# Kernel tuning notes

Measured on AMD Instinct MI355X. Metric: run time of the kernel, lower is better.

## Reference

```python
import jax, jax.numpy as jnp
import numpy as np
from jax import lax

B, N, H, L, K = 16, 2000, 128, 3, 5
LN_EPS = 1e-5


def setup_inputs() -> dict:
    key = jax.random.key(0)
    ks = jax.random.split(key, 4)
    node_emb = jax.random.normal(ks[0], (B, N, H), dtype=jnp.float32)
    dist_matrix = jax.random.uniform(ks[1], (B, N, N), dtype=jnp.float32)
    Ws = jax.random.normal(ks[2], (L, H, H), dtype=jnp.float32) / np.sqrt(H)
    bs = jax.random.normal(ks[3], (L, H), dtype=jnp.float32) * 0.02
    gammas = jnp.ones((L, H), dtype=jnp.float32)
    betas = jnp.zeros((L, H), dtype=jnp.float32)
    return {"node_emb": node_emb, "dist_matrix": dist_matrix,
            "Ws": Ws, "bs": bs, "gammas": gammas, "betas": betas}


def _layer_norm(x, gamma, beta):
    mu = jnp.mean(x, axis=-1, keepdims=True)
    var = jnp.mean(jnp.square(x - mu), axis=-1, keepdims=True)
    return (x - mu) * lax.rsqrt(var + LN_EPS) * gamma + beta


def reference(node_emb, dist_matrix, Ws, bs, gammas, betas):
    # kNN mask: k smallest distances per row (B, N, K)
    _, knn_idx = lax.top_k(-dist_matrix, K)
    b_ix = jnp.arange(B)[:, None, None]
    n_ix = jnp.arange(N)[None, :, None]
    knn_mask = jnp.zeros((B, N, N), dtype=bool).at[b_ix, n_ix, knn_idx].set(True)
    scores = jnp.where(knn_mask, -dist_matrix, -jnp.inf)
    weights = jax.nn.softmax(scores, axis=-1)  # (B, N, N)

    h = node_emb
    for l in range(L):
        agg = jnp.einsum('bnm,bmh->bnh', weights, h)
        delta = jax.nn.relu(agg @ Ws[l].T + bs[l])
        h = _layer_norm(h + delta, gammas[l], betas[l])
    return h
```

## Files before the change

kernel.cpp:

```cpp
#include <hip/hip_runtime.h>
#include <hip/hip_bf16.h>

#define BATCH 16
#define NNODE 2000
#define HDIM  128
#define KNN   5
#define NROWS (BATCH * NNODE)
#define LN_EPS 1e-5f

typedef __attribute__((ext_vector_type(8))) short short8;
typedef __attribute__((ext_vector_type(4))) float f32x4;

__global__ __launch_bounds__(256) void prep_w_kernel(
    const float* __restrict__ Ws, __hip_bfloat16* __restrict__ WB)
{
    int t = blockIdx.x * 256 + threadIdx.x;
    if (t >= 3 * 2048) return;
    int l    = t >> 11;
    int r    = t & 2047;
    int lane = r & 63;
    int ks   = (r >> 6) & 3;
    int ct   = (r >> 8) & 1;
    int wv   = (r >> 9) & 3;
    int col  = wv * 32 + ct * 16 + (lane & 15);
    int k0   = ks * 32 + (lane >> 4) * 8;
    const float* src = Ws + ((size_t)l << 14) + col * HDIM + k0;
    __hip_bfloat16* dst = WB + ((size_t)t << 3);
    #pragma unroll
    for (int e = 0; e < 8; ++e) dst[e] = __float2bfloat16(src[e]);
}

__device__ __forceinline__ unsigned long long pack_di(float v, unsigned int idx) {
    unsigned int b = __float_as_uint(v);
    b = (b & 0x80000000u) ? ~b : (b | 0x80000000u);
    return ((unsigned long long)b << 32) | idx;
}

__global__ __launch_bounds__(256) void knn_softmax_kernel(
    const float* __restrict__ dist,
    int* __restrict__ w_idx,
    float* __restrict__ w_val)
{
    int row  = blockIdx.x * 4 + (threadIdx.x >> 6);
    int lane = threadIdx.x & 63;
    const float4* r4 = reinterpret_cast<const float4*>(dist + (size_t)row * NNODE);

    unsigned long long pk0 = ~0ull, pk1 = ~0ull, pk2 = ~0ull, pk3 = ~0ull, pk4 = ~0ull;

    auto ins = [&](float d, int m) {
        unsigned long long key = pack_di(d, (unsigned int)m);
        if (key < pk4) {
            pk4 = key;
            unsigned long long t;
            if (pk4 < pk3) { t = pk3; pk3 = pk4; pk4 = t; }
            if (pk3 < pk2) { t = pk2; pk2 = pk3; pk3 = t; }
            if (pk2 < pk1) { t = pk1; pk1 = pk2; pk2 = t; }
            if (pk1 < pk0) { t = pk0; pk0 = pk1; pk1 = t; }
        }
    };

    float4 v[8];
    int base7 = lane + 448;
    bool has8 = base7 < (NNODE / 4);
    #pragma unroll
    for (int i = 0; i < 7; ++i) v[i] = r4[lane + 64 * i];
    v[7] = r4[has8 ? base7 : lane];

    #pragma unroll
    for (int i = 0; i < 7; ++i) {
        int base = (lane + 64 * i) * 4;
        ins(v[i].x, base); ins(v[i].y, base + 1);
        ins(v[i].z, base + 2); ins(v[i].w, base + 3);
    }
    if (has8) {
        int base = base7 * 4;
        ins(v[7].x, base); ins(v[7].y, base + 1);
        ins(v[7].z, base + 2); ins(v[7].w, base + 3);
    }

    unsigned long long chosen[KNN];
    #pragma unroll
    for (int r = 0; r < KNN; ++r) {
        unsigned long long mn = pk0;
        #pragma unroll
        for (int off = 32; off; off >>= 1) {
            unsigned long long o = __shfl_xor(mn, off, 64);
            if (o < mn) mn = o;
        }
        if (pk0 == mn) { pk0 = pk1; pk1 = pk2; pk2 = pk3; pk3 = pk4; pk4 = ~0ull; }
        chosen[r] = mn;
    }

    if (lane == 0) {
        float d[KNN]; int ix[KNN];
        #pragma unroll
        for (int r = 0; r < KNN; ++r) {
            unsigned int ub = (unsigned int)(chosen[r] >> 32);
            ub = (ub & 0x80000000u) ? (ub ^ 0x80000000u) : ~ub;
            d[r]  = __uint_as_float(ub);
            ix[r] = (int)(chosen[r] & 0xffffffffu);
        }
        float e[KNN]; float sum = 0.f;
        #pragma unroll
        for (int r = 0; r < KNN; ++r) { e[r] = expf(d[0] - d[r]); sum += e[r]; }
        float inv = 1.f / sum;
        #pragma unroll
        for (int r = 0; r < KNN; ++r) {
            w_idx[row * KNN + r] = ix[r];
            w_val[row * KNN + r] = e[r] * inv;
        }
    }
}

__global__ __launch_bounds__(256) void layer_kernel(
    const float* __restrict__ h_in,
    const int*   __restrict__ w_idx,
    const float* __restrict__ w_val,
    const __hip_bfloat16* __restrict__ WB,
    const float* __restrict__ bias,
    const float* __restrict__ gamma,
    const float* __restrict__ beta,
    float* __restrict__ h_out)
{
    __shared__ __hip_bfloat16 aggb[16][HDIM];
    __shared__ int   sidx[16][KNN];
    __shared__ float sw[16][KNN];
    __shared__ float wred[4][16][2];

    int tid = threadIdx.x;
    int wv  = tid >> 6;
    int l   = tid & 63;

    int bid = blockIdx.x;
    int x   = bid & 7;
    int j   = bid >> 3;
    int hi  = (j >= 125);
    int bsw = 2 * x + hi;
    int gid = bsw * 125 + (j - hi * 125);

    int node0 = gid * 16;
    size_t hbase = (size_t)bsw * NNODE * HDIM;

    const short8* wb = reinterpret_cast<const short8*>(WB);
    short8 bfrag[2][4];
    #pragma unroll
    for (int ct = 0; ct < 2; ++ct)
        #pragma unroll
        for (int ks = 0; ks < 4; ++ks)
            bfrag[ct][ks] = wb[((wv * 2 + ct) * 4 + ks) * 64 + l];

    if (tid < 16 * KNN) {
        int m = tid / KNN, k = tid % KNN;
        sidx[m][k] = w_idx[(node0 + m) * KNN + k];
        sw[m][k]   = w_val[(node0 + m) * KNN + k];
    }
    __syncthreads();

    {
        int m  = tid >> 4;
        int c0 = (tid & 15) * 8;
        float a0=0,a1=0,a2=0,a3=0,a4=0,a5=0,a6=0,a7=0;
        #pragma unroll
        for (int k = 0; k < KNN; ++k) {
            float wk = sw[m][k];
            const float4* p = reinterpret_cast<const float4*>(
                h_in + hbase + (size_t)sidx[m][k] * HDIM + c0);
            float4 v0 = p[0], v1 = p[1];
            a0 = fmaf(wk, v0.x, a0); a1 = fmaf(wk, v0.y, a1);
            a2 = fmaf(wk, v0.z, a2); a3 = fmaf(wk, v0.w, a3);
            a4 = fmaf(wk, v1.x, a4); a5 = fmaf(wk, v1.y, a5);
            a6 = fmaf(wk, v1.z, a6); a7 = fmaf(wk, v1.w, a7);
        }
        float vv[8] = {a0,a1,a2,a3,a4,a5,a6,a7};
        short8 pk;
        #pragma unroll
        for (int e = 0; e < 8; ++e) {
            __hip_bfloat16 hb = __float2bfloat16(vv[e]);
            pk[e] = *reinterpret_cast<short*>(&hb);
        }
        *reinterpret_cast<short8*>(&aggb[m][c0]) = pk;
    }
    __syncthreads();

    f32x4 acc0 = {0.f,0.f,0.f,0.f}, acc1 = {0.f,0.f,0.f,0.f};
    #pragma unroll
    for (int ks = 0; ks < 4; ++ks) {
        short8 afrag = *reinterpret_cast<const short8*>(&aggb[l & 15][ks * 32 + (l >> 4) * 8]);
        acc0 = __builtin_amdgcn_mfma_f32_16x16x32_bf16(afrag, bfrag[0][ks], acc0, 0, 0, 0);
        acc1 = __builtin_amdgcn_mfma_f32_16x16x32_bf16(afrag, bfrag[1][ks], acc1, 0, 0, 0);
    }

    int g = l >> 4;
    int col0 = wv * 32 + (l & 15);
    int col1 = col0 + 16;
    float b0  = bias[col0],  b1  = bias[col1];
    float gm0 = gamma[col0], gm1 = gamma[col1];
    float bt0 = beta[col0],  bt1 = beta[col1];

    float y0[4], y1[4];
    #pragma unroll
    for (int r = 0; r < 4; ++r) {
        int row = node0 + g * 4 + r;
        float h0 = h_in[(size_t)row * HDIM + col0];
        float h1 = h_in[(size_t)row * HDIM + col1];
        y0[r] = h0 + fmaxf(acc0[r] + b0, 0.f);
        y1[r] = h1 + fmaxf(acc1[r] + b1, 0.f);
    }

    #pragma unroll
    for (int r = 0; r < 4; ++r) {
        float ss = y0[r] + y1[r];
        float qq = y0[r] * y0[r] + y1[r] * y1[r];
        #pragma unroll
        for (int off = 1; off < 16; off <<= 1) {
            ss += __shfl_xor(ss, off, 64);
            qq += __shfl_xor(qq, off, 64);
        }
        if ((l & 15) == 0) { wred[wv][g * 4 + r][0] = ss; wred[wv][g * 4 + r][1] = qq; }
    }
    __syncthreads();

    #pragma unroll
    for (int r = 0; r < 4; ++r) {
        int row = g * 4 + r;
        float S = wred[0][row][0] + wred[1][row][0] + wred[2][row][0] + wred[3][row][0];
        float Q = wred[0][row][1] + wred[1][row][1] + wred[2][row][1] + wred[3][row][1];
        float mu  = S * (1.f / 128.f);
        float var = Q * (1.f / 128.f) - mu * mu;
        float rs  = rsqrtf(var + LN_EPS);
        size_t orow = (size_t)(node0 + row) * HDIM;
        h_out[orow + col0] = (y0[r] - mu) * rs * gm0 + bt0;
        h_out[orow + col1] = (y1[r] - mu) * rs * gm1 + bt1;
    }
}

extern "C" void kernel_launch(void* const* d_in, const int* in_sizes, int n_in,
                              void* d_out, int out_size, void* d_ws, size_t ws_size,
                              hipStream_t stream) {
    const float* node_emb = (const float*)d_in[0];
    const float* dist     = (const float*)d_in[1];
    const float* Ws       = (const float*)d_in[2];
    const float* bs       = (const float*)d_in[3];
    const float* gammas   = (const float*)d_in[4];
    const float* betas    = (const float*)d_in[5];
    float* out = (float*)d_out;

    char* ws = (char*)d_ws;
    int*   w_idx = (int*)  (ws + 0);
    float* w_val = (float*)(ws + 640000);
    __hip_bfloat16* WB = (__hip_bfloat16*)(ws + 1280000);
    float* h_mid = (float*)(ws + 1378304);

    prep_w_kernel<<<24, 256, 0, stream>>>(Ws, WB);
    knn_softmax_kernel<<<NROWS / 4, 256, 0, stream>>>(dist, w_idx, w_val);

    const int nblocks = NROWS / 16;
    const int WL = 16384;
    layer_kernel<<<nblocks, 256, 0, stream>>>(node_emb, w_idx, w_val,
        WB,          bs,           gammas,           betas,           out);
    layer_kernel<<<nblocks, 256, 0, stream>>>(out,      w_idx, w_val,
        WB + WL,     bs + HDIM,    gammas + HDIM,    betas + HDIM,    h_mid);
    layer_kernel<<<nblocks, 256, 0, stream>>>(h_mid,    w_idx, w_val,
        WB + 2*WL,   bs + 2*HDIM,  gammas + 2*HDIM,  betas + 2*HDIM,  out);
}
```

Before: 110.3 us.

## Fuse kNN softmax selection into first layer kernel and stage own rows in LDS

The separate kNN/softmax kernel is merged into the first layer kernel: each block computes top-k weights for its 16 rows, keeps them in shared memory and still writes them out for later layers. This removes one launch and the global round trip of indices and weights before layer 1. The residual rows are also loaded once, coalesced, into shared memory instead of strided global reads in the epilogue. In exchange, each wave now processes four distance rows serially, which may reduce memory parallelism on the dominant distance-matrix read, and shared memory use grows.

```diff
diff --git a/kernel.cpp b/kernel.cpp
--- a/kernel.cpp
+++ b/kernel.cpp
@@ -36,79 +36,199 @@
     return ((unsigned long long)b << 32) | idx;
 }
 
-__global__ __launch_bounds__(256) void knn_softmax_kernel(
+__global__ __launch_bounds__(256) void fused_knn_layer1_kernel(
     const float* __restrict__ dist,
-    int* __restrict__ w_idx,
-    float* __restrict__ w_val)
+    const float* __restrict__ h_in,
+    const __hip_bfloat16* __restrict__ WB0,
+    const float* __restrict__ bias,
+    const float* __restrict__ gamma,
+    const float* __restrict__ beta,
+    int*   __restrict__ w_idx,
+    float* __restrict__ w_val,
+    float* __restrict__ h_out)
 {
-    int row  = blockIdx.x * 4 + (threadIdx.x >> 6);
-    int lane = threadIdx.x & 63;
-    const float4* r4 = reinterpret_cast<const float4*>(dist + (size_t)row * NNODE);
-
-    unsigned long long pk0 = ~0ull, pk1 = ~0ull, pk2 = ~0ull, pk3 = ~0ull, pk4 = ~0ull;
-
-    auto ins = [&](float d, int m) {
-        unsigned long long key = pack_di(d, (unsigned int)m);
-        if (key < pk4) {
-            pk4 = key;
-            unsigned long long t;
-            if (pk4 < pk3) { t = pk3; pk3 = pk4; pk4 = t; }
-            if (pk3 < pk2) { t = pk2; pk2 = pk3; pk3 = t; }
-            if (pk2 < pk1) { t = pk1; pk1 = pk2; pk2 = t; }
-            if (pk1 < pk0) { t = pk0; pk0 = pk1; pk1 = t; }
-        }
-    };
-
-    float4 v[8];
-    int base7 = lane + 448;
-    bool has8 = base7 < (NNODE / 4);
-    #pragma unroll
-    for (int i = 0; i < 7; ++i) v[i] = r4[lane + 64 * i];
-    v[7] = r4[has8 ? base7 : lane];
-
-    #pragma unroll
-    for (int i = 0; i < 7; ++i) {
-        int base = (lane + 64 * i) * 4;
-        ins(v[i].x, base); ins(v[i].y, base + 1);
-        ins(v[i].z, base + 2); ins(v[i].w, base + 3);
-    }
-    if (has8) {
-        int base = base7 * 4;
-        ins(v[7].x, base); ins(v[7].y, base + 1);
-        ins(v[7].z, base + 2); ins(v[7].w, base + 3);
-    }
-
-    unsigned long long chosen[KNN];
-    #pragma unroll
-    for (int r = 0; r < KNN; ++r) {
-        unsigned long long mn = pk0;
-        #pragma unroll
-        for (int off = 32; off; off >>= 1) {
-            unsigned long long o = __shfl_xor(mn, off, 64);
-            if (o < mn) mn = o;
-        }
-        if (pk0 == mn) { pk0 = pk1; pk1 = pk2; pk2 = pk3; pk3 = pk4; pk4 = ~0ull; }
-        chosen[r] = mn;
-    }
-
-    if (lane == 0) {
-        float d[KNN]; int ix[KNN];
+    __shared__ __hip_bfloat16 aggb[16][HDIM];
+    __shared__ float hown[16][HDIM];
+    __shared__ int   sidx[16][KNN];
+    __shared__ float sw[16][KNN];
+    __shared__ float wred[4][16][2];
+
+    int tid = threadIdx.x;
+    int wv  = tid >> 6;
+    int l   = tid & 63;
+
+    int bid = blockIdx.x;
+    int x   = bid & 7;
+    int j   = bid >> 3;
+    int hi  = (j >= 125);
+    int bsw = 2 * x + hi;
+    int gid = bsw * 125 + (j - hi * 125);
+
+    int node0 = gid * 16;
+    size_t hbase = (size_t)bsw * NNODE * HDIM;
+
+    for (int rr = 0; rr < 4; ++rr) {
+        int m   = wv * 4 + rr;
+        int row = node0 + m;
+        const float4* r4 = reinterpret_cast<const float4*>(dist + (size_t)row * NNODE);
+
+        unsigned long long pk0=~0ull, pk1=~0ull, pk2=~0ull, pk3=~0ull, pk4=~0ull;
+        auto ins = [&](float d, int mm) {
+            unsigned long long key = pack_di(d, (unsigned int)mm);
+            if (key < pk4) {
+                pk4 = key;
+                unsigned long long t;
+                if (pk4 < pk3) { t = pk3; pk3 = pk4; pk4 = t; }
+                if (pk3 < pk2) { t = pk2; pk2 = pk3; pk3 = t; }
+                if (pk2 < pk1) { t = pk1; pk1 = pk2; pk2 = t; }
+                if (pk1 < pk0) { t = pk0; pk0 = pk1; pk1 = t; }
+            }
+        };
+
+        float4 v[8];
+        int base7 = l + 448;
+        bool has8 = base7 < (NNODE / 4);
+        #pragma unroll
+        for (int i = 0; i < 7; ++i) v[i] = r4[l + 64 * i];
+        v[7] = r4[has8 ? base7 : l];
+
+        #pragma unroll
+        for (int i = 0; i < 7; ++i) {
+            int base = (l + 64 * i) * 4;
+            ins(v[i].x, base); ins(v[i].y, base + 1);
+            ins(v[i].z, base + 2); ins(v[i].w, base + 3);
+        }
+        if (has8) {
+            int base = base7 * 4;
+            ins(v[7].x, base); ins(v[7].y, base + 1);
+            ins(v[7].z, base + 2); ins(v[7].w, base + 3);
+        }
+
+        unsigned long long chosen[KNN];
         #pragma unroll
         for (int r = 0; r < KNN; ++r) {
-            unsigned int ub = (unsigned int)(chosen[r] >> 32);
-            ub = (ub & 0x80000000u) ? (ub ^ 0x80000000u) : ~ub;
-            d[r]  = __uint_as_float(ub);
-            ix[r] = (int)(chosen[r] & 0xffffffffu);
-        }
-        float e[KNN]; float sum = 0.f;
-        #pragma unroll
-        for (int r = 0; r < KNN; ++r) { e[r] = expf(d[0] - d[r]); sum += e[r]; }
-        float inv = 1.f / sum;
-        #pragma unroll
-        for (int r = 0; r < KNN; ++r) {
-            w_idx[row * KNN + r] = ix[r];
-            w_val[row * KNN + r] = e[r] * inv;
-        }
+            unsigned long long mn = pk0;
+            #pragma unroll
+            for (int off = 32; off; off >>= 1) {
+                unsigned long long o = __shfl_xor(mn, off, 64);
+                if (o < mn) mn = o;
+            }
+            if (pk0 == mn) { pk0 = pk1; pk1 = pk2; pk2 = pk3; pk3 = pk4; pk4 = ~0ull; }
+            chosen[r] = mn;
+        }
+
+        if (l == 0) {
+            float d[KNN]; int ix[KNN];
+            #pragma unroll
+            for (int r = 0; r < KNN; ++r) {
+                unsigned int ub = (unsigned int)(chosen[r] >> 32);
+                ub = (ub & 0x80000000u) ? (ub ^ 0x80000000u) : ~ub;
+                d[r]  = __uint_as_float(ub);
+                ix[r] = (int)(chosen[r] & 0xffffffffu);
+            }
+            float e[KNN]; float sum = 0.f;
+            #pragma unroll
+            for (int r = 0; r < KNN; ++r) { e[r] = expf(d[0] - d[r]); sum += e[r]; }
+            float inv = 1.f / sum;
+            #pragma unroll
+            for (int r = 0; r < KNN; ++r) {
+                float wt = e[r] * inv;
+                sidx[m][r] = ix[r];
+                sw[m][r]   = wt;
+                w_idx[row * KNN + r] = ix[r];
+                w_val[row * KNN + r] = wt;
+            }
+        }
+    }
+    __syncthreads();
+
+    const short8* wb = reinterpret_cast<const short8*>(WB0);
+    short8 bfrag[2][4];
+    #pragma unroll
+    for (int ct = 0; ct < 2; ++ct)
+        #pragma unroll
+        for (int ks = 0; ks < 4; ++ks)
+            bfrag[ct][ks] = wb[((wv * 2 + ct) * 4 + ks) * 64 + l];
+
+    {
+        int m  = tid >> 4;
+        int c0 = (tid & 15) * 8;
+        const float4* po = reinterpret_cast<const float4*>(
+            h_in + (size_t)(node0 + m) * HDIM + c0);
+        float4 o0 = po[0], o1 = po[1];
+        *reinterpret_cast<float4*>(&hown[m][c0])     = o0;
+        *reinterpret_cast<float4*>(&hown[m][c0 + 4]) = o1;
+
+        float a0=0,a1=0,a2=0,a3=0,a4=0,a5=0,a6=0,a7=0;
+        #pragma unroll
+        for (int k = 0; k < KNN; ++k) {
+            float wk = sw[m][k];
+            const float4* p = reinterpret_cast<const float4*>(
+                h_in + hbase + (size_t)sidx[m][k] * HDIM + c0);
+            float4 v0 = p[0], v1 = p[1];
+            a0 = fmaf(wk, v0.x, a0); a1 = fmaf(wk, v0.y, a1);
+            a2 = fmaf(wk, v0.z, a2); a3 = fmaf(wk, v0.w, a3);
+            a4 = fmaf(wk, v1.x, a4); a5 = fmaf(wk, v1.y, a5);
+            a6 = fmaf(wk, v1.z, a6); a7 = fmaf(wk, v1.w, a7);
+        }
+        float vv[8] = {a0,a1,a2,a3,a4,a5,a6,a7};
+        short8 pk;
+        #pragma unroll
+        for (int e = 0; e < 8; ++e) {
+            __hip_bfloat16 hb = __float2bfloat16(vv[e]);
+            pk[e] = *reinterpret_cast<short*>(&hb);
+        }
+        *reinterpret_cast<short8*>(&aggb[m][c0]) = pk;
+    }
+    __syncthreads();
+
+    f32x4 acc0 = {0.f,0.f,0.f,0.f}, acc1 = {0.f,0.f,0.f,0.f};
+    #pragma unroll
+    for (int ks = 0; ks < 4; ++ks) {
+        short8 afrag = *reinterpret_cast<const short8*>(&aggb[l & 15][ks * 32 + (l >> 4) * 8]);
+        acc0 = __builtin_amdgcn_mfma_f32_16x16x32_bf16(afrag, bfrag[0][ks], acc0, 0, 0, 0);
+        acc1 = __builtin_amdgcn_mfma_f32_16x16x32_bf16(afrag, bfrag[1][ks], acc1, 0, 0, 0);
+    }
+
+    int g = l >> 4;
+    int col0 = wv * 32 + (l & 15);
+    int col1 = col0 + 16;
+    float b0  = bias[col0],  b1  = bias[col1];
+    float gm0 = gamma[col0], gm1 = gamma[col1];
+    float bt0 = beta[col0],  bt1 = beta[col1];
+
+    float y0[4], y1[4];
+    #pragma unroll
+    for (int r = 0; r < 4; ++r) {
+        int rl = g * 4 + r;
+        y0[r] = hown[rl][col0] + fmaxf(acc0[r] + b0, 0.f);
+        y1[r] = hown[rl][col1] + fmaxf(acc1[r] + b1, 0.f);
+    }
+
+    #pragma unroll
+    for (int r = 0; r < 4; ++r) {
+        float ss = y0[r] + y1[r];
+        float qq = y0[r] * y0[r] + y1[r] * y1[r];
+        #pragma unroll
+        for (int off = 1; off < 16; off <<= 1) {
+            ss += __shfl_xor(ss, off, 64);
+            qq += __shfl_xor(qq, off, 64);
+        }
+        if ((l & 15) == 0) { wred[wv][g * 4 + r][0] = ss; wred[wv][g * 4 + r][1] = qq; }
+    }
+    __syncthreads();
+
+    #pragma unroll
+    for (int r = 0; r < 4; ++r) {
+        int row = g * 4 + r;
+        float S = wred[0][row][0] + wred[1][row][0] + wred[2][row][0] + wred[3][row][0];
+        float Q = wred[0][row][1] + wred[1][row][1] + wred[2][row][1] + wred[3][row][1];
+        float mu  = S * (1.f / 128.f);
+        float var = Q * (1.f / 128.f) - mu * mu;
+        float rs  = rsqrtf(var + LN_EPS);
+        size_t orow = (size_t)(node0 + row) * HDIM;
+        h_out[orow + col0] = (y0[r] - mu) * rs * gm0 + bt0;
+        h_out[orow + col1] = (y1[r] - mu) * rs * gm1 + bt1;
     }
 }
 
@@ -123,6 +243,7 @@
     float* __restrict__ h_out)
 {
     __shared__ __hip_bfloat16 aggb[16][HDIM];
+    __shared__ float hown[16][HDIM];
     __shared__ int   sidx[16][KNN];
     __shared__ float sw[16][KNN];
     __shared__ float wred[4][16][2];
@@ -159,6 +280,12 @@
     {
         int m  = tid >> 4;
         int c0 = (tid & 15) * 8;
+        const float4* po = reinterpret_cast<const float4*>(
+            h_in + (size_t)(node0 + m) * HDIM + c0);
+        float4 o0 = po[0], o1 = po[1];
+        *reinterpret_cast<float4*>(&hown[m][c0])     = o0;
+        *reinterpret_cast<float4*>(&hown[m][c0 + 4]) = o1;
+
         float a0=0,a1=0,a2=0,a3=0,a4=0,a5=0,a6=0,a7=0;
         #pragma unroll
         for (int k = 0; k < KNN; ++k) {
@@ -200,11 +327,9 @@
     float y0[4], y1[4];
     #pragma unroll
     for (int r = 0; r < 4; ++r) {
-        int row = node0 + g * 4 + r;
-        float h0 = h_in[(size_t)row * HDIM + col0];
-        float h1 = h_in[(size_t)row * HDIM + col1];
-        y0[r] = h0 + fmaxf(acc0[r] + b0, 0.f);
-        y1[r] = h1 + fmaxf(acc1[r] + b1, 0.f);
+        int rl = g * 4 + r;
+        y0[r] = hown[rl][col0] + fmaxf(acc0[r] + b0, 0.f);
+        y1[r] = hown[rl][col1] + fmaxf(acc1[r] + b1, 0.f);
     }
 
     #pragma unroll
@@ -252,14 +377,15 @@
     float* h_mid = (float*)(ws + 1378304);
 
     prep_w_kernel<<<24, 256, 0, stream>>>(Ws, WB);
-    knn_softmax_kernel<<<NROWS / 4, 256, 0, stream>>>(dist, w_idx, w_val);
 
     const int nblocks = NROWS / 16;
     const int WL = 16384;
-    layer_kernel<<<nblocks, 256, 0, stream>>>(node_emb, w_idx, w_val,
-        WB,          bs,           gammas,           betas,           out);
-    layer_kernel<<<nblocks, 256, 0, stream>>>(out,      w_idx, w_val,
-        WB + WL,     bs + HDIM,    gammas + HDIM,    betas + HDIM,    h_mid);
-    layer_kernel<<<nblocks, 256, 0, stream>>>(h_mid,    w_idx, w_val,
-        WB + 2*WL,   bs + 2*HDIM,  gammas + 2*HDIM,  betas + 2*HDIM,  out);
-}
+
+    fused_knn_layer1_kernel<<<nblocks, 256, 0, stream>>>(
+        dist, node_emb, WB, bs, gammas, betas, w_idx, w_val, out);
+
+    layer_kernel<<<nblocks, 256, 0, stream>>>(out,   w_idx, w_val,
+        WB + WL,   bs + HDIM,   gammas + HDIM,   betas + HDIM,   h_mid);
+    layer_kernel<<<nblocks, 256, 0, stream>>>(h_mid, w_idx, w_val,
+        WB + 2*WL, bs + 2*HDIM, gammas + 2*HDIM, betas + 2*HDIM, out);
+}
```

Measured after the change: 124.2 us. +12.6%, slower.

## Store intermediate node features in bf16 and fuse weight/embedding prep into kNN kernel

Applied to the files above, without the earlier changes.

Converts node embeddings to bf16 in the kNN kernel and keeps inter-layer hidden states in bf16, halving gather and store traffic in each layer kernel. The residual input is staged in shared memory from the already-loaded own row instead of re-read from global memory. The weight-prep kernel is merged into the kNN launch. The residual path and intermediate layer-norm outputs lose precision because of bf16 storage.

```diff
diff --git a/kernel.cpp b/kernel.cpp
--- a/kernel.cpp
+++ b/kernel.cpp
@@ -11,23 +11,13 @@
 typedef __attribute__((ext_vector_type(8))) short short8;
 typedef __attribute__((ext_vector_type(4))) float f32x4;
 
-__global__ __launch_bounds__(256) void prep_w_kernel(
-    const float* __restrict__ Ws, __hip_bfloat16* __restrict__ WB)
-{
-    int t = blockIdx.x * 256 + threadIdx.x;
-    if (t >= 3 * 2048) return;
-    int l    = t >> 11;
-    int r    = t & 2047;
-    int lane = r & 63;
-    int ks   = (r >> 6) & 3;
-    int ct   = (r >> 8) & 1;
-    int wv   = (r >> 9) & 3;
-    int col  = wv * 32 + ct * 16 + (lane & 15);
-    int k0   = ks * 32 + (lane >> 4) * 8;
-    const float* src = Ws + ((size_t)l << 14) + col * HDIM + k0;
-    __hip_bfloat16* dst = WB + ((size_t)t << 3);
-    #pragma unroll
-    for (int e = 0; e < 8; ++e) dst[e] = __float2bfloat16(src[e]);
+__device__ __forceinline__ float b2f(short s) {
+    unsigned int u = ((unsigned int)(unsigned short)s) << 16;
+    return __uint_as_float(u);
+}
+__device__ __forceinline__ short f2b(float f) {
+    __hip_bfloat16 h = __float2bfloat16(f);
+    return *reinterpret_cast<short*>(&h);
 }
 
 __device__ __forceinline__ unsigned long long pack_di(float v, unsigned int idx) {
@@ -36,11 +26,41 @@
     return ((unsigned long long)b << 32) | idx;
 }
 
-__global__ __launch_bounds__(256) void knn_softmax_kernel(
+__global__ __launch_bounds__(256) void knn_prep_kernel(
     const float* __restrict__ dist,
+    const float* __restrict__ Ws,
+    const float* __restrict__ node_emb,
+    __hip_bfloat16* __restrict__ WB,
+    short* __restrict__ hb,
     int* __restrict__ w_idx,
     float* __restrict__ w_val)
 {
+    int tg = blockIdx.x * 256 + threadIdx.x;
+
+    if (tg < 3 * 2048) {
+        int l    = tg >> 11;
+        int r    = tg & 2047;
+        int lane = r & 63;
+        int ks   = (r >> 6) & 3;
+        int ct   = (r >> 8) & 1;
+        int wv   = (r >> 9) & 3;
+        int col  = wv * 32 + ct * 16 + (lane & 15);
+        int k0   = ks * 32 + (lane >> 4) * 8;
+        const float* src = Ws + ((size_t)l << 14) + col * HDIM + k0;
+        __hip_bfloat16* dst = WB + ((size_t)tg << 3);
+        #pragma unroll
+        for (int e = 0; e < 8; ++e) dst[e] = __float2bfloat16(src[e]);
+    }
+
+    if (tg < NROWS * HDIM / 8) {
+        const float4* src = reinterpret_cast<const float4*>(node_emb) + tg * 2;
+        float4 a = src[0], bq = src[1];
+        short8 pk;
+        pk[0]=f2b(a.x); pk[1]=f2b(a.y); pk[2]=f2b(a.z); pk[3]=f2b(a.w);
+        pk[4]=f2b(bq.x); pk[5]=f2b(bq.y); pk[6]=f2b(bq.z); pk[7]=f2b(bq.w);
+        *reinterpret_cast<short8*>(hb + (size_t)tg * 8) = pk;
+    }
+
     int row  = blockIdx.x * 4 + (threadIdx.x >> 6);
     int lane = threadIdx.x & 63;
     const float4* r4 = reinterpret_cast<const float4*>(dist + (size_t)row * NNODE);
@@ -112,17 +132,20 @@
     }
 }
 
-__global__ __launch_bounds__(256) void layer_kernel(
-    const float* __restrict__ h_in,
+template<bool OUT_F32>
+__global__ __launch_bounds__(256) void layer_kernel_b(
+    const short* __restrict__ hin,
     const int*   __restrict__ w_idx,
     const float* __restrict__ w_val,
     const __hip_bfloat16* __restrict__ WB,
     const float* __restrict__ bias,
     const float* __restrict__ gamma,
     const float* __restrict__ beta,
-    float* __restrict__ h_out)
+    short* __restrict__ hout_b,
+    float* __restrict__ hout_f)
 {
     __shared__ __hip_bfloat16 aggb[16][HDIM];
+    __shared__ short hown[16][HDIM];
     __shared__ int   sidx[16][KNN];
     __shared__ float sw[16][KNN];
     __shared__ float wred[4][16][2];
@@ -159,26 +182,25 @@
     {
         int m  = tid >> 4;
         int c0 = (tid & 15) * 8;
+        short8 own = *reinterpret_cast<const short8*>(
+            hin + (size_t)(node0 + m) * HDIM + c0);
+        *reinterpret_cast<short8*>(&hown[m][c0]) = own;
+
         float a0=0,a1=0,a2=0,a3=0,a4=0,a5=0,a6=0,a7=0;
         #pragma unroll
         for (int k = 0; k < KNN; ++k) {
             float wk = sw[m][k];
-            const float4* p = reinterpret_cast<const float4*>(
-                h_in + hbase + (size_t)sidx[m][k] * HDIM + c0);
-            float4 v0 = p[0], v1 = p[1];
-            a0 = fmaf(wk, v0.x, a0); a1 = fmaf(wk, v0.y, a1);
-            a2 = fmaf(wk, v0.z, a2); a3 = fmaf(wk, v0.w, a3);
-            a4 = fmaf(wk, v1.x, a4); a5 = fmaf(wk, v1.y, a5);
-            a6 = fmaf(wk, v1.z, a6); a7 = fmaf(wk, v1.w, a7);
-        }
-        float vv[8] = {a0,a1,a2,a3,a4,a5,a6,a7};
+            short8 hv = *reinterpret_cast<const short8*>(
+                hin + hbase + (size_t)sidx[m][k] * HDIM + c0);
+            a0 = fmaf(wk, b2f(hv[0]), a0); a1 = fmaf(wk, b2f(hv[1]), a1);
+            a2 = fmaf(wk, b2f(hv[2]), a2); a3 = fmaf(wk, b2f(hv[3]), a3);
+            a4 = fmaf(wk, b2f(hv[4]), a4); a5 = fmaf(wk, b2f(hv[5]), a5);
+            a6 = fmaf(wk, b2f(hv[6]), a6); a7 = fmaf(wk, b2f(hv[7]), a7);
+        }
         short8 pk;
-        #pragma unroll
-        for (int e = 0; e < 8; ++e) {
-            __hip_bfloat16 hb = __float2bfloat16(vv[e]);
-            pk[e] = *reinterpret_cast<short*>(&hb);
-        }
-        *reinterpret_cast<short8*>(&aggb[m][c0]) = pk;
+        pk[0]=f2b(a0); pk[1]=f2b(a1); pk[2]=f2b(a2); pk[3]=f2b(a3);
+        pk[4]=f2b(a4); pk[5]=f2b(a5); pk[6]=f2b(a6); pk[7]=f2b(a7);
+        *reinterpret_cast<short8*>(&aggb[tid >> 4][c0]) = pk;
     }
     __syncthreads();
 
@@ -200,11 +222,9 @@
     float y0[4], y1[4];
     #pragma unroll
     for (int r = 0; r < 4; ++r) {
-        int row = node0 + g * 4 + r;
-        float h0 = h_in[(size_t)row * HDIM + col0];
-        float h1 = h_in[(size_t)row * HDIM + col1];
-        y0[r] = h0 + fmaxf(acc0[r] + b0, 0.f);
-        y1[r] = h1 + fmaxf(acc1[r] + b1, 0.f);
+        int rl = g * 4 + r;
+        y0[r] = b2f(hown[rl][col0]) + fmaxf(acc0[r] + b0, 0.f);
+        y1[r] = b2f(hown[rl][col1]) + fmaxf(acc1[r] + b1, 0.f);
     }
 
     #pragma unroll
@@ -229,8 +249,15 @@
         float var = Q * (1.f / 128.f) - mu * mu;
         float rs  = rsqrtf(var + LN_EPS);
         size_t orow = (size_t)(node0 + row) * HDIM;
-        h_out[orow + col0] = (y0[r] - mu) * rs * gm0 + bt0;
-        h_out[orow + col1] = (y1[r] - mu) * rs * gm1 + bt1;
+        float o0 = (y0[r] - mu) * rs * gm0 + bt0;
+        float o1 = (y1[r] - mu) * rs * gm1 + bt1;
+        if (OUT_F32) {
+            hout_f[orow + col0] = o0;
+            hout_f[orow + col1] = o1;
+        } else {
+            hout_b[orow + col0] = f2b(o0);
+            hout_b[orow + col1] = f2b(o1);
+        }
     }
 }
 
@@ -249,17 +276,20 @@
     int*   w_idx = (int*)  (ws + 0);
     float* w_val = (float*)(ws + 640000);
     __hip_bfloat16* WB = (__hip_bfloat16*)(ws + 1280000);
-    float* h_mid = (float*)(ws + 1378304);
-
-    prep_w_kernel<<<24, 256, 0, stream>>>(Ws, WB);
-    knn_softmax_kernel<<<NROWS / 4, 256, 0, stream>>>(dist, w_idx, w_val);
+    short* hb  = (short*)(ws + 1378304);
+    short* h1b = (short*)(ws + 9570304);
+    short* h2b = (short*)(ws + 17762304);
+
+    knn_prep_kernel<<<NROWS / 4, 256, 0, stream>>>(
+        dist, Ws, node_emb, WB, hb, w_idx, w_val);
 
     const int nblocks = NROWS / 16;
     const int WL = 16384;
-    layer_kernel<<<nblocks, 256, 0, stream>>>(node_emb, w_idx, w_val,
-        WB,          bs,           gammas,           betas,           out);
-    layer_kernel<<<nblocks, 256, 0, stream>>>(out,      w_idx, w_val,
-        WB + WL,     bs + HDIM,    gammas + HDIM,    betas + HDIM,    h_mid);
-    layer_kernel<<<nblocks, 256, 0, stream>>>(h_mid,    w_idx, w_val,
-        WB + 2*WL,   bs + 2*HDIM,  gammas + 2*HDIM,  betas + 2*HDIM,  out);
-}
+
+    layer_kernel_b<false><<<nblocks, 256, 0, stream>>>(hb,  w_idx, w_val,
+        WB,        bs,          gammas,          betas,          h1b, nullptr);
+    layer_kernel_b<false><<<nblocks, 256, 0, stream>>>(h1b, w_idx, w_val,
+        WB + WL,   bs + HDIM,   gammas + HDIM,   betas + HDIM,   h2b, nullptr);
+    layer_kernel_b<true><<<nblocks, 256, 0, stream>>>(h2b, w_idx, w_val,
+        WB + 2*WL, bs + 2*HDIM, gammas + 2*HDIM, betas + 2*HDIM, nullptr, out);
+}
```

Result: faster. 102.3 us (-7.3%).
